# Performance work log

Measured on AMD Instinct MI355X. Metric: run time of the kernel, lower is better.

The kernel has to match this reference:

```python
import jax, jax.numpy as jnp
import numpy as np
import math

N_HEAD = 8


def _rope(x):
    # x: [B, H, S, D]; lucidrains rotary_embedding_torch default: interleaved pairs, theta=10000
    D = x.shape[-1]
    S = x.shape[-2]
    inv_freq = 1.0 / (10000.0 ** (jnp.arange(0, D, 2, dtype=jnp.float32) / D))  # [D/2]
    t = jnp.arange(S, dtype=jnp.float32)
    freqs = jnp.repeat(t[:, None] * inv_freq[None, :], 2, axis=-1)  # [S, D] interleaved repeat
    cos = jnp.cos(freqs).astype(x.dtype)
    sin = jnp.sin(freqs).astype(x.dtype)
    xp = x.reshape(*x.shape[:-1], D // 2, 2)
    rot = jnp.stack((-xp[..., 1], xp[..., 0]), axis=-1).reshape(x.shape)  # rotate_half (interleaved)
    return x * cos + rot * sin


def _row_linear(x, Wo):
    # faithful RowLinear: transpose then flat-reshape back (a real permutation), linear, inverse shuffle
    B, S, P = x.shape
    E = Wo.shape[0]
    x = jnp.swapaxes(x, 1, 2).reshape(B, S, P)
    x = jnp.einsum('bsp,ep->bse', x, Wo)  # [B, S, E]
    x = x.reshape(B, E, -1)  # [B, E, S]
    return jnp.swapaxes(x, 1, 2)  # [B, S, E]


def setup_inputs() -> dict:
    key = jax.random.key(0)
    k0, k1, k2, k3, k4 = jax.random.split(key, 5)
    B, S, E, P = 4, 2048, 1024, 1024
    std = 1.0 / math.sqrt(E)
    return {
        'emb': jax.random.normal(k0, (B, S, E), dtype=jnp.float32),
        'W1': jax.random.normal(k1, (P, E), dtype=jnp.float32) * std,
        'W2': jax.random.normal(k2, (P, E), dtype=jnp.float32) * std,
        'W3': jax.random.normal(k3, (P, E), dtype=jnp.float32) * std,
        'Wo': jax.random.normal(k4, (E, P), dtype=jnp.float32) * std,
    }


def reference(emb, W1, W2, W3, Wo):
    B, S, E = emb.shape
    P = W1.shape[0]
    H = N_HEAD
    D = P // H
    q = jnp.einsum('bse,pe->bsp', emb, W1).reshape(B, H, S, D)  # raw view split (as in source)
    k = jnp.einsum('bse,pe->bsp', emb, W2).reshape(B, H, S, D)
    v = jnp.einsum('bse,pe->bsp', emb, W3).reshape(B, H, S, D)
    q = _rope(q)
    k = _rope(k)
    scores = jnp.einsum('bhqd,bhkd->bhqk', q, k).astype(jnp.float32) / math.sqrt(H)
    attn = jax.nn.softmax(scores, axis=-1).astype(v.dtype)
    out = jnp.einsum('bhqk,bhkd->bhqd', attn, v)  # [B, H, S, D]
    out = jnp.swapaxes(out, 1, 2).reshape(B, S, P)
    return _row_linear(out, Wo)
```

## Files before the change

kernel.cpp:

```cpp
#include <hip/hip_runtime.h>

typedef float f32x4 __attribute__((ext_vector_type(4)));
typedef __bf16 bf16x8 __attribute__((ext_vector_type(8)));

__device__ __forceinline__ unsigned short f2bf(float f) {
  unsigned int u = __float_as_uint(f);
  u = (u + 0x7FFFu + ((u >> 16) & 1u)) >> 16;
  return (unsigned short)u;
}

__device__ __forceinline__ f32x4 mfma16(bf16x8 a, bf16x8 b, f32x4 c) {
  return __builtin_amdgcn_mfma_f32_16x16x32_bf16(a, b, c, 0, 0, 0);
}

__device__ __forceinline__ void load8_bf16(const unsigned short* p, unsigned short* d) {
  *(uint4*)d = *(const uint4*)p;
}
__device__ __forceinline__ void load8_bf16(const float* p, unsigned short* d) {
  float4 a = *(const float4*)p;
  float4 b = *(const float4*)(p + 4);
  __align__(16) unsigned short t[8] = {f2bf(a.x), f2bf(a.y), f2bf(a.z), f2bf(a.w),
                                       f2bf(b.x), f2bf(b.y), f2bf(b.z), f2bf(b.w)};
  *(uint4*)d = *(uint4*)t;
}

__global__ __launch_bounds__(256) void gemm_qkv(const float* __restrict__ A,
                                                const float* __restrict__ W1,
                                                const float* __restrict__ W2,
                                                const float* __restrict__ W3,
                                                unsigned short* __restrict__ q,
                                                unsigned short* __restrict__ k,
                                                unsigned short* __restrict__ v) {
  __shared__ __align__(16) unsigned short As[128][40];
  __shared__ __align__(16) unsigned short Bs[128][40];
  const int t = threadIdx.x;
  const int lane = t & 63;
  const int wid = t >> 6;
  const int quad = lane >> 4;
  const int l16 = lane & 15;
  const int wm = (wid >> 1) << 6;
  const int wn = (wid & 1) << 6;
  const int sel = blockIdx.x >> 3;
  const int nb = (blockIdx.x & 7) << 7;
  const int mbase = blockIdx.y * 128;
  const float* Bt = (sel == 0) ? W1 : (sel == 1) ? W2 : W3;
  unsigned short* C = (sel == 0) ? q : (sel == 1) ? k : v;

  f32x4 acc[4][4] = {};

  for (int k0 = 0; k0 < 1024; k0 += 32) {
#pragma unroll
    for (int i = 0; i < 2; ++i) {
      int c = t + (i << 8);
      int row = c >> 2;
      int col = (c & 3) << 3;
      load8_bf16(A + (size_t)(mbase + row) * 1024 + k0 + col, &As[row][col]);
      load8_bf16(Bt + (size_t)(nb + row) * 1024 + k0 + col, &Bs[row][col]);
    }
    __syncthreads();
    bf16x8 af[4], bfr[4];
#pragma unroll
    for (int mt = 0; mt < 4; ++mt)
      af[mt] = *(const bf16x8*)(&As[wm + mt * 16 + l16][quad * 8]);
#pragma unroll
    for (int nt = 0; nt < 4; ++nt)
      bfr[nt] = *(const bf16x8*)(&Bs[wn + nt * 16 + l16][quad * 8]);
#pragma unroll
    for (int mt = 0; mt < 4; ++mt)
#pragma unroll
      for (int nt = 0; nt < 4; ++nt)
        acc[mt][nt] = mfma16(af[mt], bfr[nt], acc[mt][nt]);
    __syncthreads();
  }

  const bool rope = (sel < 2);
#pragma unroll
  for (int mt = 0; mt < 4; ++mt) {
#pragma unroll
    for (int nt = 0; nt < 4; ++nt) {
#pragma unroll
      for (int r = 0; r < 4; ++r) {
        int row_g = mbase + wm + mt * 16 + quad * 4 + r;
        int col_g = nb + wn + nt * 16 + l16;
        float val = acc[mt][nt][r];
        if (rope) {
          float other = __shfl_xor(val, 1);
          int s = (((row_g & 2047) << 3) + (col_g >> 7)) & 2047;
          int d = col_g & 127;
          float invf = __expf(-0.14391156f * (float)(d >> 1));
          float ang = (float)s * invf;
          float sv, cv;
          __sincosf(ang, &sv, &cv);
          val = (d & 1) ? (val * cv + other * sv) : (val * cv - other * sv);
        }
        C[(size_t)row_g * 1024 + col_g] = f2bf(val);
      }
    }
  }
}

__global__ __launch_bounds__(256) void transpose_v(const unsigned short* __restrict__ Vn,
                                                   unsigned short* __restrict__ VT) {
  __shared__ __align__(16) unsigned short tile[64][72];
  const int t = threadIdx.x;
  const int s0 = blockIdx.x * 64;
  const int d0 = blockIdx.y * 64;
  const int bh = blockIdx.z;
  const size_t base = (size_t)bh * (2048 * 128);
#pragma unroll
  for (int i = 0; i < 2; ++i) {
    int c = t + (i << 8);
    int sr = c >> 3;
    int dc = (c & 7) << 3;
    *(uint4*)(&tile[sr][dc]) = *(const uint4*)(Vn + base + (size_t)(s0 + sr) * 128 + d0 + dc);
  }
  __syncthreads();
#pragma unroll
  for (int i = 0; i < 2; ++i) {
    int c = t + (i << 8);
    int dr = c >> 3;
    int sc = (c & 7) << 3;
    __align__(16) unsigned short tmp[8];
#pragma unroll
    for (int j = 0; j < 8; ++j) tmp[j] = tile[sc + j][dr];
    *(uint4*)(VT + base + (size_t)(d0 + dr) * 2048 + s0 + sc) = *(uint4*)tmp;
  }
}

__global__ __launch_bounds__(256) void gemm_out(const unsigned short* __restrict__ OT,
                                                const float* __restrict__ Bt,
                                                float* __restrict__ C) {
  __shared__ __align__(16) char smem_raw[128 * 68 * 4];
  auto As = (unsigned short(*)[40])smem_raw;
  auto Bs = (unsigned short(*)[40])(smem_raw + 128 * 40 * 2);
  const int t = threadIdx.x;
  const int lane = t & 63;
  const int wid = t >> 6;
  const int quad = lane >> 4;
  const int l16 = lane & 15;
  const int wm = (wid >> 1) << 6;
  const int wn = (wid & 1) << 6;
  const int mbase = blockIdx.y * 128;
  const int nbase = blockIdx.x * 128;

  f32x4 acc[4][4] = {};

  for (int k0 = 0; k0 < 1024; k0 += 32) {
#pragma unroll
    for (int i = 0; i < 2; ++i) {
      int c = t + (i << 8);
      int row = c >> 2;
      int col = (c & 3) << 3;
      int R = mbase + row;
      int b = R >> 11;
      int ii = R & 2047;
      const unsigned short* src = OT + (size_t)(b * 8 + (ii >> 8)) * (128 * 2048) +
                                  (size_t)((ii >> 1) & 127) * 2048 + ((ii & 1) << 10) +
                                  k0 + col;
      load8_bf16(src, &As[row][col]);
      load8_bf16(Bt + (size_t)(nbase + row) * 1024 + k0 + col, &Bs[row][col]);
    }
    __syncthreads();
    bf16x8 af[4], bfr[4];
#pragma unroll
    for (int mt = 0; mt < 4; ++mt)
      af[mt] = *(const bf16x8*)(&As[wm + mt * 16 + l16][quad * 8]);
#pragma unroll
    for (int nt = 0; nt < 4; ++nt)
      bfr[nt] = *(const bf16x8*)(&Bs[wn + nt * 16 + l16][quad * 8]);
#pragma unroll
    for (int mt = 0; mt < 4; ++mt)
#pragma unroll
      for (int nt = 0; nt < 4; ++nt)
        acc[mt][nt] = mfma16(af[mt], bfr[nt], acc[mt][nt]);
    __syncthreads();
  }

  float(*Ts)[68] = (float(*)[68])smem_raw;
  const int b = mbase >> 11;
  const int ebase = (mbase & 2047) >> 1;
#pragma unroll
  for (int p = 0; p < 2; ++p) {
    __syncthreads();
#pragma unroll
    for (int mt = 0; mt < 4; ++mt)
#pragma unroll
      for (int nt = 0; nt < 4; ++nt)
#pragma unroll
        for (int rr = p; rr < 4; rr += 2) {
          int col_local = wn + nt * 16 + l16;
          int row_local = wm + mt * 16 + quad * 4 + rr;
          Ts[col_local][row_local >> 1] = acc[mt][nt][rr];
        }
    __syncthreads();
    int srow = t >> 1;
    int e0 = (t & 1) << 5;
    float* dst = C + (size_t)b * 2097152 +
                 (size_t)(p * 1024 + nbase + srow) * 1024 + ebase + e0;
#pragma unroll
    for (int j = 0; j < 8; ++j)
      ((float4*)dst)[j] = *(const float4*)&Ts[srow][e0 + j * 4];
  }
}

__global__ __launch_bounds__(256, 2) void flash_attn(const unsigned short* __restrict__ Q,
                                                     const unsigned short* __restrict__ Kg,
                                                     const unsigned short* __restrict__ VTg,
                                                     unsigned short* __restrict__ OT) {
  __shared__ __align__(16) char sm[54272];
  auto Ks = (unsigned short(*)[136])sm;
  auto Vt = (unsigned short(*)[72])(sm + 17408);
  auto Ps = (unsigned short(*)[32][72])(sm + 35840);
  const int t = threadIdx.x;
  const int lane = t & 63;
  const int wid = t >> 6;
  const int quad = lane >> 4;
  const int l16 = lane & 15;
  const int i = blockIdx.x;
  const int bh = (i & 7) + ((i >> 3) & 3) * 8;
  const int qbase = (i >> 5) << 7;
  const size_t base = (size_t)bh * (2048 * 128);
  const float scale = 0.3535533905932738f;

  bf16x8 qf[2][4];
#pragma unroll
  for (int mt = 0; mt < 2; ++mt) {
    int row = qbase + wid * 32 + mt * 16 + l16;
#pragma unroll
    for (int ks = 0; ks < 4; ++ks)
      qf[mt][ks] = *(const bf16x8*)(Q + base + (size_t)row * 128 + ks * 32 + quad * 8);
  }

  f32x4 accO[2][8] = {};
  float mst[2][4], lst[2][4];
#pragma unroll
  for (int mt = 0; mt < 2; ++mt)
#pragma unroll
    for (int r = 0; r < 4; ++r) { mst[mt][r] = -__builtin_inff(); lst[mt][r] = 0.f; }

  for (int kv0 = 0; kv0 < 2048; kv0 += 64) {
#pragma unroll
    for (int i2 = 0; i2 < 4; ++i2) {
      int c = t + (i2 << 8);
      int row = c >> 4;
      int col = (c & 15) << 3;
      *(uint4*)(&Ks[row][col]) = *(const uint4*)(Kg + base + (size_t)(kv0 + row) * 128 + col);
    }
#pragma unroll
    for (int i2 = 0; i2 < 4; ++i2) {
      int c = t + (i2 << 8);
      int row = c >> 3;
      int col = (c & 7) << 3;
      *(uint4*)(&Vt[row][col]) =
          *(const uint4*)(VTg + base + (size_t)row * 2048 + kv0 + col);
    }
    __syncthreads();

    f32x4 accS[2][4];
#pragma unroll
    for (int nt = 0; nt < 4; ++nt) {
      bf16x8 kf[4];
#pragma unroll
      for (int ks = 0; ks < 4; ++ks)
        kf[ks] = *(const bf16x8*)(&Ks[nt * 16 + l16][ks * 32 + quad * 8]);
#pragma unroll
      for (int mt = 0; mt < 2; ++mt) {
        f32x4 a = {0.f, 0.f, 0.f, 0.f};
#pragma unroll
        for (int ks = 0; ks < 4; ++ks)
          a = mfma16(qf[mt][ks], kf[ks], a);
        accS[mt][nt] = a;
      }
    }

#pragma unroll
    for (int mt = 0; mt < 2; ++mt) {
#pragma unroll
      for (int r = 0; r < 4; ++r) {
        float mx = fmaxf(fmaxf(accS[mt][0][r], accS[mt][1][r]),
                         fmaxf(accS[mt][2][r], accS[mt][3][r]));
#pragma unroll
        for (int off = 1; off < 16; off <<= 1) mx = fmaxf(mx, __shfl_xor(mx, off));
        float mnew = fmaxf(mst[mt][r], mx);
        float alpha = __expf((mst[mt][r] - mnew) * scale);
        float negms = -mnew * scale;
        float psum = 0.f;
#pragma unroll
        for (int nt = 0; nt < 4; ++nt) {
          float p = __expf(fmaf(accS[mt][nt][r], scale, negms));
          accS[mt][nt][r] = p;
          psum += p;
        }
#pragma unroll
        for (int off = 1; off < 16; off <<= 1) psum += __shfl_xor(psum, off);
        lst[mt][r] = lst[mt][r] * alpha + psum;
        mst[mt][r] = mnew;
#pragma unroll
        for (int dt = 0; dt < 8; ++dt) accO[mt][dt][r] *= alpha;
      }
    }

#pragma unroll
    for (int mt = 0; mt < 2; ++mt)
#pragma unroll
      for (int nt = 0; nt < 4; ++nt)
#pragma unroll
        for (int r = 0; r < 4; ++r)
          Ps[wid][mt * 16 + quad * 4 + r][nt * 16 + l16] = f2bf(accS[mt][nt][r]);

    bf16x8 pf[2][2];
#pragma unroll
    for (int mt = 0; mt < 2; ++mt)
#pragma unroll
      for (int ks = 0; ks < 2; ++ks)
        pf[mt][ks] = *(const bf16x8*)(&Ps[wid][mt * 16 + l16][ks * 32 + quad * 8]);
#pragma unroll
    for (int dt = 0; dt < 8; ++dt) {
      bf16x8 vf[2];
#pragma unroll
      for (int ks = 0; ks < 2; ++ks)
        vf[ks] = *(const bf16x8*)(&Vt[dt * 16 + l16][ks * 32 + quad * 8]);
#pragma unroll
      for (int mt = 0; mt < 2; ++mt)
#pragma unroll
        for (int ks = 0; ks < 2; ++ks)
          accO[mt][dt] = mfma16(pf[mt][ks], vf[ks], accO[mt][dt]);
    }
    __syncthreads();
  }

  auto To = (unsigned short(*)[136])sm;
#pragma unroll
  for (int mt = 0; mt < 2; ++mt) {
#pragma unroll
    for (int r = 0; r < 4; ++r) {
      float inv = 1.f / lst[mt][r];
      int srow = wid * 32 + mt * 16 + quad * 4 + r;
#pragma unroll
      for (int dt = 0; dt < 8; ++dt)
        To[dt * 16 + l16][srow] = f2bf(accO[mt][dt][r] * inv);
    }
  }
  __syncthreads();
  int dr = t >> 1;
  int off = (t & 1) << 6;
  unsigned short* dst = OT + base + (size_t)dr * 2048 + qbase + off;
#pragma unroll
  for (int j = 0; j < 8; ++j)
    ((uint4*)dst)[j] = *(const uint4*)&To[dr][off + j * 8];
}

extern "C" void kernel_launch(void* const* d_in, const int* in_sizes, int n_in,
                              void* d_out, int out_size, void* d_ws, size_t ws_size,
                              hipStream_t stream) {
  const float* emb = (const float*)d_in[0];
  const float* W1  = (const float*)d_in[1];
  const float* W2  = (const float*)d_in[2];
  const float* W3  = (const float*)d_in[3];
  const float* Wo  = (const float*)d_in[4];
  float* out = (float*)d_out;

  const size_t NELEM = (size_t)8 * 1024 * 1024;
  unsigned short* q  = (unsigned short*)d_ws;
  unsigned short* k  = q + NELEM;
  unsigned short* vn = k + NELEM;
  unsigned short* vT = vn + NELEM;
  unsigned short* oT = vn;

  dim3 blk(256, 1, 1);
  gemm_qkv<<<dim3(24, 64), blk, 0, stream>>>(emb, W1, W2, W3, q, k, vn);
  transpose_v<<<dim3(32, 2, 32), blk, 0, stream>>>(vn, vT);
  flash_attn<<<dim3(512, 1, 1), blk, 0, stream>>>(q, k, vT, oT);
  gemm_out<<<dim3(8, 64), blk, 0, stream>>>(oT, Wo, out);
}
```

Baseline: 392.6 us.

## Pre-convert weights and embeddings to bf16; compute softmax row sums with MFMA

Adds conversion kernels that turn W1/W2/W3, Wo and (when the workspace is large enough) emb into bf16 once per call, so the GEMMs load half as many bytes and skip per-tile fp32-to-bf16 conversion. In flash attention, the per-row shuffle reduction of the softmax denominator is replaced by an MFMA of P against a ones vector. This adds extra kernel launches and a full read/write pass over the inputs. It also sums the bf16-rounded probabilities instead of the fp32 ones.

```diff
diff --git a/kernel.cpp b/kernel.cpp
--- a/kernel.cpp
+++ b/kernel.cpp
@@ -24,10 +24,30 @@
   *(uint4*)d = *(uint4*)t;
 }
 
-__global__ __launch_bounds__(256) void gemm_qkv(const float* __restrict__ A,
-                                                const float* __restrict__ W1,
-                                                const float* __restrict__ W2,
-                                                const float* __restrict__ W3,
+__global__ __launch_bounds__(256) void convert_gen(const float* __restrict__ src,
+                                                   unsigned short* __restrict__ dst) {
+  int idx = (blockIdx.x * 256 + threadIdx.x) * 8;
+  __align__(16) unsigned short t[8];
+  load8_bf16(src + idx, t);
+  *(uint4*)(dst + idx) = *(uint4*)t;
+}
+
+__global__ __launch_bounds__(256) void convert_w3(const float* __restrict__ W1,
+                                                  const float* __restrict__ W2,
+                                                  const float* __restrict__ W3,
+                                                  unsigned short* __restrict__ dst) {
+  int i = blockIdx.x;
+  int sel = i >> 9;
+  const float* src = (sel == 0) ? W1 : (sel == 1) ? W2 : W3;
+  int off = (i & 511) * 2048 + threadIdx.x * 8;
+  __align__(16) unsigned short t[8];
+  load8_bf16(src + off, t);
+  *(uint4*)(dst + sel * 1048576 + off) = *(uint4*)t;
+}
+
+template <typename TA>
+__global__ __launch_bounds__(256) void gemm_qkv(const TA* __restrict__ A,
+                                                const unsigned short* __restrict__ WB,
                                                 unsigned short* __restrict__ q,
                                                 unsigned short* __restrict__ k,
                                                 unsigned short* __restrict__ v) {
@@ -43,7 +63,7 @@
   const int sel = blockIdx.x >> 3;
   const int nb = (blockIdx.x & 7) << 7;
   const int mbase = blockIdx.y * 128;
-  const float* Bt = (sel == 0) ? W1 : (sel == 1) ? W2 : W3;
+  const unsigned short* Bt = WB + sel * 1048576;
   unsigned short* C = (sel == 0) ? q : (sel == 1) ? k : v;
 
   f32x4 acc[4][4] = {};
@@ -128,7 +148,7 @@
 }
 
 __global__ __launch_bounds__(256) void gemm_out(const unsigned short* __restrict__ OT,
-                                                const float* __restrict__ Bt,
+                                                const unsigned short* __restrict__ Bt,
                                                 float* __restrict__ C) {
   __shared__ __align__(16) char smem_raw[128 * 68 * 4];
   auto As = (unsigned short(*)[40])smem_raw;
@@ -222,6 +242,10 @@
   const size_t base = (size_t)bh * (2048 * 128);
   const float scale = 0.3535533905932738f;
 
+  bf16x8 ones8;
+#pragma unroll
+  for (int j = 0; j < 8; ++j) ones8[j] = (__bf16)1.0f;
+
   bf16x8 qf[2][4];
 #pragma unroll
   for (int mt = 0; mt < 2; ++mt) {
@@ -232,11 +256,12 @@
   }
 
   f32x4 accO[2][8] = {};
-  float mst[2][4], lst[2][4];
+  f32x4 accL[2] = {};
+  float mst[2][4];
 #pragma unroll
   for (int mt = 0; mt < 2; ++mt)
 #pragma unroll
-    for (int r = 0; r < 4; ++r) { mst[mt][r] = -__builtin_inff(); lst[mt][r] = 0.f; }
+    for (int r = 0; r < 4; ++r) mst[mt][r] = -__builtin_inff();
 
   for (int kv0 = 0; kv0 < 2048; kv0 += 64) {
 #pragma unroll
@@ -284,17 +309,11 @@
         float mnew = fmaxf(mst[mt][r], mx);
         float alpha = __expf((mst[mt][r] - mnew) * scale);
         float negms = -mnew * scale;
-        float psum = 0.f;
-#pragma unroll
-        for (int nt = 0; nt < 4; ++nt) {
-          float p = __expf(fmaf(accS[mt][nt][r], scale, negms));
-          accS[mt][nt][r] = p;
-          psum += p;
-        }
-#pragma unroll
-        for (int off = 1; off < 16; off <<= 1) psum += __shfl_xor(psum, off);
-        lst[mt][r] = lst[mt][r] * alpha + psum;
+#pragma unroll
+        for (int nt = 0; nt < 4; ++nt)
+          accS[mt][nt][r] = __expf(fmaf(accS[mt][nt][r], scale, negms));
         mst[mt][r] = mnew;
+        accL[mt][r] *= alpha;
 #pragma unroll
         for (int dt = 0; dt < 8; ++dt) accO[mt][dt][r] *= alpha;
       }
@@ -314,6 +333,13 @@
 #pragma unroll
       for (int ks = 0; ks < 2; ++ks)
         pf[mt][ks] = *(const bf16x8*)(&Ps[wid][mt * 16 + l16][ks * 32 + quad * 8]);
+
+#pragma unroll
+    for (int mt = 0; mt < 2; ++mt)
+#pragma unroll
+      for (int ks = 0; ks < 2; ++ks)
+        accL[mt] = mfma16(pf[mt][ks], ones8, accL[mt]);
+
 #pragma unroll
     for (int dt = 0; dt < 8; ++dt) {
       bf16x8 vf[2];
@@ -334,7 +360,7 @@
   for (int mt = 0; mt < 2; ++mt) {
 #pragma unroll
     for (int r = 0; r < 4; ++r) {
-      float inv = 1.f / lst[mt][r];
+      float inv = 1.f / accL[mt][r];
       int srow = wid * 32 + mt * 16 + quad * 4 + r;
 #pragma unroll
       for (int dt = 0; dt < 8; ++dt)
@@ -361,15 +387,28 @@
   float* out = (float*)d_out;
 
   const size_t NELEM = (size_t)8 * 1024 * 1024;
-  unsigned short* q  = (unsigned short*)d_ws;
-  unsigned short* k  = q + NELEM;
-  unsigned short* vn = k + NELEM;
-  unsigned short* vT = vn + NELEM;
-  unsigned short* oT = vn;
+  unsigned short* q    = (unsigned short*)d_ws;
+  unsigned short* k    = q + NELEM;
+  unsigned short* vn   = k + NELEM;
+  unsigned short* X    = vn + NELEM;
+  unsigned short* oT   = vn;
+  unsigned short* vT   = X;
+  unsigned short* W123B = X;
+  unsigned short* WoB  = X;
+  unsigned short* embB = X + NELEM * 2;
+
+  const bool use_embB = ws_size >= (size_t)80 * 1024 * 1024;
 
   dim3 blk(256, 1, 1);
-  gemm_qkv<<<dim3(24, 64), blk, 0, stream>>>(emb, W1, W2, W3, q, k, vn);
+  convert_w3<<<dim3(1536), blk, 0, stream>>>(W1, W2, W3, W123B);
+  if (use_embB) {
+    convert_gen<<<dim3(4096), blk, 0, stream>>>(emb, embB);
+    gemm_qkv<unsigned short><<<dim3(24, 64), blk, 0, stream>>>(embB, W123B, q, k, vn);
+  } else {
+    gemm_qkv<float><<<dim3(24, 64), blk, 0, stream>>>(emb, W123B, q, k, vn);
+  }
   transpose_v<<<dim3(32, 2, 32), blk, 0, stream>>>(vn, vT);
   flash_attn<<<dim3(512, 1, 1), blk, 0, stream>>>(q, k, vT, oT);
-  gemm_out<<<dim3(8, 64), blk, 0, stream>>>(oT, Wo, out);
-}
+  convert_gen<<<dim3(512), blk, 0, stream>>>(Wo, WoB);
+  gemm_out<<<dim3(8, 64), blk, 0, stream>>>(oT, WoB, out);
+}
```

Measured after the change: 366.2 us. 1.07x faster.
